# Kernel tuning notes

Measured on AMD Instinct MI355X. Metric: run time of the kernel, lower is better.

The kernel has to match this reference:

```python
import jax, jax.numpy as jnp
import numpy as np

POOL_SIZE = 7


def setup_inputs() -> dict:
    key = jax.random.key(0)
    k1, k2, k3 = jax.random.split(key, 3)
    B, H, W, C = 1, 128, 128, 1024
    N = 512
    shared_layers = jax.random.normal(k1, (B, H, W, C), dtype=jnp.float32)
    # Build valid boxes [ymin, xmin, ymax, xmax] with min <= max, inside the map.
    mins = jax.random.uniform(k2, (N, 2), minval=0.0, maxval=float(H - 2))
    spans = jax.random.uniform(k3, (N, 2), minval=1.0, maxval=32.0)
    maxs = jnp.minimum(mins + spans, float(H - 1))
    rois = jnp.stack([mins[:, 0], mins[:, 1], maxs[:, 0], maxs[:, 1]], axis=1).astype(jnp.float32)
    return {"shared_layers": shared_layers, "rois": rois}


def reference(shared_layers, rois):
    """Per-ROI crop + bilinear resize (TF1 resize_bilinear, align_corners=False),
    concatenated over ROIs then flattened. Fully vectorized over ROIs."""
    P = POOL_SIZE
    B, H, W, C = shared_layers.shape  # B == 1 as in the original usage
    feat = shared_layers[0]  # [H, W, C]

    ymin = rois[:, 0].astype(jnp.int32)
    xmin = rois[:, 1].astype(jnp.int32)
    ymax = rois[:, 2].astype(jnp.int32)
    xmax = rois[:, 3].astype(jnp.int32)
    h = (ymax - ymin + 1).astype(jnp.float32)  # [N]
    w = (xmax - xmin + 1).astype(jnp.float32)

    grid = jnp.arange(P, dtype=jnp.float32)  # [P]
    # TF resize_bilinear (align_corners=False): src = out_idx * in_size / out_size
    src_y = grid[None, :] * (h[:, None] / P)  # [N, P]
    src_x = grid[None, :] * (w[:, None] / P)  # [N, P]

    y0 = jnp.floor(src_y).astype(jnp.int32)
    x0 = jnp.floor(src_x).astype(jnp.int32)
    y1 = jnp.minimum(y0 + 1, (ymax - ymin)[:, None])
    x1 = jnp.minimum(x0 + 1, (xmax - xmin)[:, None])
    fy = (src_y - y0.astype(jnp.float32))[:, :, None, None]  # [N, P, 1, 1]
    fx = (src_x - x0.astype(jnp.float32))[:, None, :, None]  # [N, 1, P, 1]

    gy0 = ymin[:, None] + y0  # [N, P] global row indices
    gy1 = ymin[:, None] + y1
    gx0 = xmin[:, None] + x0  # [N, P] global col indices
    gx1 = xmin[:, None] + x1

    # 4 corner gathers -> [N, P, P, C]
    tl = feat[gy0[:, :, None], gx0[:, None, :]]
    tr = feat[gy0[:, :, None], gx1[:, None, :]]
    bl = feat[gy1[:, :, None], gx0[:, None, :]]
    br = feat[gy1[:, :, None], gx1[:, None, :]]

    top = tl + (tr - tl) * fx
    bot = bl + (br - bl) * fx
    out = top + (bot - top) * fy  # [N, P, P, C]

    return out.reshape(out.shape[0], -1)  # Flatten -> [N, P*P*C]
```

## Files before the change

### kernel.cpp

```cpp
#include <hip/hip_runtime.h>


#define POOL_P 7
#define FEAT_C 1024
#define FEAT_W 128
#define CELLS_PER_ROI (POOL_P * POOL_P)
#define GROUP_BLOCKS  (8 * CELLS_PER_ROI)

typedef float vfloat4 __attribute__((ext_vector_type(4)));

__global__ __launch_bounds__(128) void roi_pool_kernel(
    const float* __restrict__ feat,
    const float* __restrict__ rois,
    float* __restrict__ out)
{
    const int i    = blockIdx.x;
    const int q    = i / GROUP_BLOCKS;
    const int k    = i - q * GROUP_BLOCKS;
    const int r    = 8 * q + (k & 7);
    const int cell = k >> 3;
    const int px   = cell % POOL_P;
    const int py   = cell / POOL_P;

    const float4 roi = ((const float4*)rois)[r];
    const int ymin = (int)roi.x;
    const int xmin = (int)roi.y;
    const int ymax = (int)roi.z;
    const int xmax = (int)roi.w;

    const float h = (float)(ymax - ymin + 1);
    const float w = (float)(xmax - xmin + 1);

    const float src_y = (float)py * (h / 7.0f);
    const float src_x = (float)px * (w / 7.0f);

    const int y0 = (int)floorf(src_y);
    const int x0 = (int)floorf(src_x);
    const int y1 = min(y0 + 1, ymax - ymin);
    const int x1 = min(x0 + 1, xmax - xmin);

    const float fy = src_y - (float)y0;
    const float fx = src_x - (float)x0;

    const bool nx = (x1 != x0) && (fx != 0.0f);
    const bool ny = (y1 != y0) && (fy != 0.0f);

    const int gy0 = ymin + y0;
    const int gy1 = ymin + y1;
    const int gx0 = xmin + x0;
    const int gx1 = xmin + x1;

    const float4* __restrict__ tlp = (const float4*)(feat + ((size_t)(gy0 * FEAT_W + gx0)) * FEAT_C);
    const float4* __restrict__ trp = (const float4*)(feat + ((size_t)(gy0 * FEAT_W + gx1)) * FEAT_C);
    const float4* __restrict__ blp = (const float4*)(feat + ((size_t)(gy1 * FEAT_W + gx0)) * FEAT_C);
    const float4* __restrict__ brp = (const float4*)(feat + ((size_t)(gy1 * FEAT_W + gx1)) * FEAT_C);
    vfloat4* __restrict__ op = (vfloat4*)(out + ((size_t)r * CELLS_PER_ROI + cell) * FEAT_C);

    const int t0 = threadIdx.x;
    const int t1 = t0 + 128;

    const float4 tl0 = tlp[t0];
    const float4 tl1 = tlp[t1];
    float4 tr0, tr1, bl0, bl1, br0, br1;
    if (nx)       { tr0 = trp[t0]; tr1 = trp[t1]; }
    if (ny)       { bl0 = blp[t0]; bl1 = blp[t1]; }
    if (nx && ny) { br0 = brp[t0]; br1 = brp[t1]; }

    if (!nx) { tr0 = tl0; tr1 = tl1; }
    if (!ny) { bl0 = tl0; bl1 = tl1; }
    if (!(nx && ny)) {
        br0 = (!nx) ? bl0 : tr0;
        br1 = (!nx) ? bl1 : tr1;
    }

    vfloat4 res0, res1;
    {
        float top, bot;
        top = tl0.x + (tr0.x - tl0.x) * fx; bot = bl0.x + (br0.x - bl0.x) * fx; res0.x = top + (bot - top) * fy;
        top = tl0.y + (tr0.y - tl0.y) * fx; bot = bl0.y + (br0.y - bl0.y) * fx; res0.y = top + (bot - top) * fy;
        top = tl0.z + (tr0.z - tl0.z) * fx; bot = bl0.z + (br0.z - bl0.z) * fx; res0.z = top + (bot - top) * fy;
        top = tl0.w + (tr0.w - tl0.w) * fx; bot = bl0.w + (br0.w - bl0.w) * fx; res0.w = top + (bot - top) * fy;
        top = tl1.x + (tr1.x - tl1.x) * fx; bot = bl1.x + (br1.x - bl1.x) * fx; res1.x = top + (bot - top) * fy;
        top = tl1.y + (tr1.y - tl1.y) * fx; bot = bl1.y + (br1.y - bl1.y) * fx; res1.y = top + (bot - top) * fy;
        top = tl1.z + (tr1.z - tl1.z) * fx; bot = bl1.z + (br1.z - bl1.z) * fx; res1.z = top + (bot - top) * fy;
        top = tl1.w + (tr1.w - tl1.w) * fx; bot = bl1.w + (br1.w - bl1.w) * fx; res1.w = top + (bot - top) * fy;
    }

    __builtin_nontemporal_store(res0, &op[t0]);
    __builtin_nontemporal_store(res1, &op[t1]);
}

extern "C" void kernel_launch(void* const* d_in, const int* in_sizes, int n_in,
                              void* d_out, int out_size, void* d_ws, size_t ws_size,
                              hipStream_t stream) {
    const float* feat = (const float*)d_in[0];
    const float* rois = (const float*)d_in[1];
    float* out        = (float*)d_out;

    const int n_rois   = in_sizes[1] / 4;
    const int n_blocks = n_rois * CELLS_PER_ROI;

    roi_pool_kernel<<<n_blocks, 128, 0, stream>>>(feat, rois, out);
}
```

Before: 167.8 us.

## Sort ROIs by spatial position so nearby ROIs share cached feature rows

Adds a single-block bitonic sort that orders ROIs by (ymin, xmin) and writes a permutation to workspace. The pooling kernel then processes ROIs in that order, so ROIs running at the same time tend to overlap in the feature map and reuse data in L2/MALL. The cost is an extra serial kernel launch with many barriers before the main kernel. The sorted path only runs when there are exactly 512 ROIs and enough workspace is provided.

Measured after the change: 168.5 us. No clear change (+0.5%).

```diff
diff --git a/kernel.cpp b/kernel.cpp
--- a/kernel.cpp
+++ b/kernel.cpp
@@ -6,21 +6,51 @@
 #define FEAT_W 128
 #define CELLS_PER_ROI (POOL_P * POOL_P)
 #define GROUP_BLOCKS  (8 * CELLS_PER_ROI)
+#define N_ROIS 512
 
 typedef float vfloat4 __attribute__((ext_vector_type(4)));
+
+__global__ __launch_bounds__(N_ROIS) void roi_sort_kernel(
+    const float* __restrict__ rois, unsigned* __restrict__ perm)
+{
+    __shared__ unsigned sk[N_ROIS];
+    const int tid = threadIdx.x;
+    {
+        const float4 roi = ((const float4*)rois)[tid];
+        const unsigned ymin = (unsigned)(int)roi.x;
+        const unsigned xmin = (unsigned)(int)roi.y;
+        sk[tid] = (((ymin << 7) | xmin) << 10) | (unsigned)tid;
+    }
+    __syncthreads();
+    for (int k = 2; k <= N_ROIS; k <<= 1) {
+        for (int j = k >> 1; j > 0; j >>= 1) {
+            const int ixj = tid ^ j;
+            if (ixj > tid) {
+                const bool up = ((tid & k) == 0);
+                const unsigned a = sk[tid], b = sk[ixj];
+                if ((a > b) == up) { sk[tid] = b; sk[ixj] = a; }
+            }
+            __syncthreads();
+        }
+    }
+    perm[tid] = sk[tid] & 1023u;
+}
 
 __global__ __launch_bounds__(128) void roi_pool_kernel(
     const float* __restrict__ feat,
     const float* __restrict__ rois,
-    float* __restrict__ out)
+    float* __restrict__ out,
+    const unsigned* __restrict__ perm)
 {
-    const int i    = blockIdx.x;
-    const int q    = i / GROUP_BLOCKS;
-    const int k    = i - q * GROUP_BLOCKS;
-    const int r    = 8 * q + (k & 7);
-    const int cell = k >> 3;
-    const int px   = cell % POOL_P;
-    const int py   = cell / POOL_P;
+    const int i     = blockIdx.x;
+    const int q     = i / GROUP_BLOCKS;
+    const int k     = i - q * GROUP_BLOCKS;
+    const int rslot = 8 * q + (k & 7);
+    const int cell  = k >> 3;
+    const int px    = cell % POOL_P;
+    const int py    = cell / POOL_P;
+
+    const int r = perm ? (int)perm[rslot] : rslot;
 
     const float4 roi = ((const float4*)rois)[r];
     const int ymin = (int)roi.x;
@@ -100,5 +130,10 @@
     const int n_rois   = in_sizes[1] / 4;
     const int n_blocks = n_rois * CELLS_PER_ROI;
 
-    roi_pool_kernel<<<n_blocks, 128, 0, stream>>>(feat, rois, out);
+    unsigned* perm = nullptr;
+    if (n_rois == N_ROIS && ws_size >= N_ROIS * sizeof(unsigned)) {
+        perm = (unsigned*)d_ws;
+        roi_sort_kernel<<<1, N_ROIS, 0, stream>>>(rois, perm);
+    }
+    roi_pool_kernel<<<n_blocks, 128, 0, stream>>>(feat, rois, out, perm);
 }
```
